# Kernel optimization log

Hardware: AMD Instinct MI355X
Metric: run time of the kernel (lower is better)

Reference implementation:

```python
import jax, jax.numpy as jnp
import numpy as np

K, N, BETA, DIM = 128, 15, 0.05, 512


def _safe_dist(sq):
    # sqrt with zero (sub)gradient at 0, matching torch.cdist/norm behavior
    pos = sq > 0
    return jnp.sqrt(jnp.where(pos, sq, 1.0)) * pos


def setup_inputs() -> dict:
    key = jax.random.key(0)
    embeddings = jax.random.normal(key, (K * N, DIM), dtype=jnp.float32)
    return {"embeddings": embeddings}


def reference(embeddings) -> jnp.ndarray:
    # ---- pairwise Euclidean distance matrix (torch.cdist, p=2) ----
    sq_norms = jnp.sum(embeddings * embeddings, axis=-1)  # [KN]
    sq = sq_norms[:, None] + sq_norms[None, :] - 2.0 * (embeddings @ embeddings.T)
    pdist = _safe_dist(jnp.maximum(sq, 0.0))  # [KN, KN]

    # ---- set margin loss over all identity pairs (a < b), vectorized ----
    blocks = pdist.reshape(K, N, K, N)  # blocks[a, i, b, k] = d(x_{a,i}, x_{b,k})
    ia, ib = jnp.triu_indices(K, k=1)   # P = K*(K-1)/2 pairs
    dAA = blocks[ia, :, ia, :]          # [P, N, N] intra-set distances of set a
    dAB = blocks[ia, :, ib, :]          # [P, N, N] cross distances a -> b
    # margin[p, i, j, k] = relu(dAA[p,i,j] - dAB[p,i,k] + 1.5), masked to i < j
    margin = jnp.maximum(dAA[:, :, :, None] - dAB[:, :, None, :] + 1.5, 0.0)
    mask_ij = jnp.triu(jnp.ones((N, N), dtype=margin.dtype), k=1)  # p buffer: 1 iff i<j
    set_margin_loss = jnp.sum(margin * mask_ij[None, :, :, None])
    total_pairs = ia.shape[0]
    set_margin_loss = set_margin_loss / (N * N * (N - 1) / 2)
    set_margin_loss = set_margin_loss / total_pairs

    # ---- centroid radius penalty ----
    groups = embeddings.reshape(K, N, -1)
    centroids = jnp.mean(groups, axis=1, keepdims=True)        # [K, 1, D]
    diff = groups - centroids
    dists = _safe_dist(jnp.sum(diff * diff, axis=-1))          # [K, N]
    mean_dist = jnp.mean(dists, axis=1)                        # [K]
    total_radius = jnp.mean(mean_dist)
    radius_penalty = BETA * jnp.mean(jnp.abs(mean_dist / total_radius - 1.0))

    return set_margin_loss + radius_penalty
```

## Files before the change

kernel.cpp:

```cpp
#include <hip/hip_runtime.h>
#include <math.h>

#define M 1920
#define DIMS 512
#define KGRP 128
#define NGRP 15
#define NQ 32
#define KC 32
#define NTILES 528
#define SPAD 40

typedef __attribute__((ext_vector_type(8))) short bf16x8;
typedef __attribute__((ext_vector_type(4))) float f32x4;

#define MFMA(A, B, C) __builtin_amdgcn_mfma_f32_16x16x32_bf16(A, B, C, 0, 0, 0)

__device__ inline void split2(float x, short& h, short& l) {
    unsigned u = __float_as_uint(x);
    h = (short)(u >> 16);
    float fl = x - __uint_as_float(u & 0xFFFF0000u);
    l = (short)(__float_as_uint(fl) >> 16);
}

__global__ __launch_bounds__(256) void daa_norm_kernel(const float* __restrict__ E,
                                                       float* __restrict__ dAAg,
                                                       float* __restrict__ sqn) {
    const int a = blockIdx.x;
    const int t = threadIdx.x;
    __shared__ float Ash[NGRP][516];
    const float4* Ea = reinterpret_cast<const float4*>(E + (size_t)a * NGRP * DIMS);
    for (int e = t; e < NGRP * (DIMS / 4); e += 256) {
        int r = e / (DIMS / 4), c4 = e % (DIMS / 4);
        *reinterpret_cast<float4*>(&Ash[r][c4 * 4]) = Ea[r * (DIMS / 4) + c4];
    }
    __syncthreads();
    if (t < NGRP * NGRP) {
        int i = t / NGRP, j = t % NGRP;
        float s = 0.0f;
        #pragma unroll 4
        for (int k = 0; k < DIMS; k += 4) {
            float4 ai = *reinterpret_cast<const float4*>(&Ash[i][k]);
            float4 aj = *reinterpret_cast<const float4*>(&Ash[j][k]);
            float dx = ai.x - aj.x, dy = ai.y - aj.y, dz = ai.z - aj.z, dw = ai.w - aj.w;
            s = fmaf(dx, dx, s); s = fmaf(dy, dy, s);
            s = fmaf(dz, dz, s); s = fmaf(dw, dw, s);
        }
        dAAg[a * 225 + t] = sqrtf(s);
    } else if (t >= 240 && t < 240 + NGRP) {
        int i = t - 240;
        float s = 0.0f;
        #pragma unroll 4
        for (int k = 0; k < DIMS; k += 4) {
            float4 ai = *reinterpret_cast<const float4*>(&Ash[i][k]);
            s = fmaf(ai.x, ai.x, s); s = fmaf(ai.y, ai.y, s);
            s = fmaf(ai.z, ai.z, s); s = fmaf(ai.w, ai.w, s);
        }
        sqn[a * NGRP + i] = s;
    }
}

__global__ __launch_bounds__(256) void quad_kernel(const float* __restrict__ E,
                                                   const float* __restrict__ sqn,
                                                   const float* __restrict__ dAAg,
                                                   float* __restrict__ acc) {
    int qa = 0, rem = blockIdx.x;
    while (rem >= NQ - qa) { rem -= NQ - qa; ++qa; }
    const int qb = qa + rem;

    __shared__ short Ah[64][SPAD], Al[64][SPAD], Bh[64][SPAD], Bl[64][SPAD];
    __shared__ float Dt[64][68];
    __shared__ float dAAc[4][228];
    __shared__ float sqnA[64], sqnB[64];
    __shared__ unsigned char ijt[105][2];
    __shared__ float wred[4];

    const int t = threadIdx.x;
    const int row0 = qa * 60, col0 = qb * 60;

    for (int e = t; e < 900; e += 256)
        dAAc[e / 225][e % 225] = dAAg[(qa * 4 + e / 225) * 225 + e % 225];
    if (t < 64) {
        sqnA[t] = sqn[row0 + min(t, 59)];
        sqnB[t] = sqn[col0 + min(t, 59)];
    }
    if (t < 105) {
        int i = 0, r2 = t;
        while (r2 >= 14 - i) { r2 -= 14 - i; ++i; }
        ijt[t][0] = (unsigned char)i;
        ijt[t][1] = (unsigned char)(i + 1 + r2);
    }

    const int wv = t >> 6, lane = t & 63;
    const int lr = lane & 15, lk = (lane >> 4) * 8;

    const int srow = t >> 2;
    const int skq = (t & 3) * 8;
    const float* pA = &E[(size_t)(row0 + min(srow, 59)) * DIMS + skq];
    const float* pB = &E[(size_t)(col0 + min(srow, 59)) * DIMS + skq];

    f32x4 z4 = {0.f, 0.f, 0.f, 0.f};
    f32x4 c0 = z4, c1 = z4, c2 = z4, c3 = z4;

    for (int k0 = 0; k0 < DIMS; k0 += KC) {
        __syncthreads();
        {
            float4 va0 = *reinterpret_cast<const float4*>(pA + k0);
            float4 va1 = *reinterpret_cast<const float4*>(pA + k0 + 4);
            float4 vb0 = *reinterpret_cast<const float4*>(pB + k0);
            float4 vb1 = *reinterpret_cast<const float4*>(pB + k0 + 4);
            float xa[8] = {va0.x, va0.y, va0.z, va0.w, va1.x, va1.y, va1.z, va1.w};
            float xb[8] = {vb0.x, vb0.y, vb0.z, vb0.w, vb1.x, vb1.y, vb1.z, vb1.w};
            bf16x8 ah, al, bh, bl;
            #pragma unroll
            for (int i = 0; i < 8; ++i) {
                short h, l;
                split2(xa[i], h, l); ah[i] = h; al[i] = l;
                split2(xb[i], h, l); bh[i] = h; bl[i] = l;
            }
            *reinterpret_cast<bf16x8*>(&Ah[srow][skq]) = ah;
            *reinterpret_cast<bf16x8*>(&Al[srow][skq]) = al;
            *reinterpret_cast<bf16x8*>(&Bh[srow][skq]) = bh;
            *reinterpret_cast<bf16x8*>(&Bl[srow][skq]) = bl;
        }
        __syncthreads();
        bf16x8 a_h = *reinterpret_cast<const bf16x8*>(&Ah[(wv << 4) + lr][lk]);
        bf16x8 a_l = *reinterpret_cast<const bf16x8*>(&Al[(wv << 4) + lr][lk]);
        bf16x8 b_h0 = *reinterpret_cast<const bf16x8*>(&Bh[lr][lk]);
        bf16x8 b_l0 = *reinterpret_cast<const bf16x8*>(&Bl[lr][lk]);
        bf16x8 b_h1 = *reinterpret_cast<const bf16x8*>(&Bh[16 + lr][lk]);
        bf16x8 b_l1 = *reinterpret_cast<const bf16x8*>(&Bl[16 + lr][lk]);
        bf16x8 b_h2 = *reinterpret_cast<const bf16x8*>(&Bh[32 + lr][lk]);
        bf16x8 b_l2 = *reinterpret_cast<const bf16x8*>(&Bl[32 + lr][lk]);
        bf16x8 b_h3 = *reinterpret_cast<const bf16x8*>(&Bh[48 + lr][lk]);
        bf16x8 b_l3 = *reinterpret_cast<const bf16x8*>(&Bl[48 + lr][lk]);
        c0 = MFMA(a_l, b_h0, c0); c0 = MFMA(a_h, b_l0, c0); c0 = MFMA(a_h, b_h0, c0);
        c1 = MFMA(a_l, b_h1, c1); c1 = MFMA(a_h, b_l1, c1); c1 = MFMA(a_h, b_h1, c1);
        c2 = MFMA(a_l, b_h2, c2); c2 = MFMA(a_h, b_l2, c2); c2 = MFMA(a_h, b_h2, c2);
        c3 = MFMA(a_l, b_h3, c3); c3 = MFMA(a_h, b_l3, c3); c3 = MFMA(a_h, b_h3, c3);
    }

    {
        const int rbase = (wv << 4) + ((lane >> 4) << 2);
        #define EPI(J, CJ)                                                    \
        {   _Pragma("unroll")                                                 \
            for (int r = 0; r < 4; ++r) {                                     \
                int rr = rbase + r;                                           \
                int cc = (J << 4) + lr;                                       \
                float sq = sqnA[rr] + sqnB[cc] - 2.0f * CJ[r];                \
                Dt[rr][cc] = sqrtf(fmaxf(sq, 0.0f));                          \
            }                                                                 \
        }
        EPI(0, c0) EPI(1, c1) EPI(2, c2) EPI(3, c3)
        #undef EPI
    }
    __syncthreads();

    float v = 0.0f;
    for (int it = t; it < 16 * 105; it += 256) {
        int p16 = it / 105, r2 = it % 105;
        int pa = p16 >> 2, pb = p16 & 3;
        int a = qa * 4 + pa, b = qb * 4 + pb;
        if (a < b) {
            int i = ijt[r2][0], j = ijt[r2][1];
            float base = dAAc[pa][i * 15 + j] + 1.5f;
            const float* drow = &Dt[pa * 15 + i][pb * 15];
            #pragma unroll
            for (int l = 0; l < NGRP; ++l) v += fmaxf(base - drow[l], 0.0f);
        }
    }
    #pragma unroll
    for (int off = 32; off > 0; off >>= 1) v += __shfl_down(v, off);
    if ((t & 63) == 0) wred[t >> 6] = v;
    __syncthreads();
    if (t == 0) atomicAdd(acc, wred[0] + wred[1] + wred[2] + wred[3]);
}

__global__ __launch_bounds__(256) void radius_kernel(const float* __restrict__ E,
                                                     float* __restrict__ md) {
    const int g = blockIdx.x;
    const int t = threadIdx.x;
    __shared__ float cent[DIMS];
    __shared__ float ws4[4];
    float c0 = 0.0f, c1 = 0.0f;
    #pragma unroll
    for (int m = 0; m < NGRP; ++m) {
        c0 += E[(size_t)(g * NGRP + m) * DIMS + t];
        c1 += E[(size_t)(g * NGRP + m) * DIMS + t + 256];
    }
    cent[t]       = c0 / (float)NGRP;
    cent[t + 256] = c1 / (float)NGRP;
    __syncthreads();
    float sumd = 0.0f;
    for (int m = 0; m < NGRP; ++m) {
        float d0 = E[(size_t)(g * NGRP + m) * DIMS + t]       - cent[t];
        float d1 = E[(size_t)(g * NGRP + m) * DIMS + t + 256] - cent[t + 256];
        float v = d0 * d0 + d1 * d1;
        #pragma unroll
        for (int off = 32; off > 0; off >>= 1) v += __shfl_down(v, off);
        if ((t & 63) == 0) ws4[t >> 6] = v;
        __syncthreads();
        if (t == 0) {
            float s = ws4[0] + ws4[1] + ws4[2] + ws4[3];
            sumd += (s > 0.0f) ? sqrtf(s) : 0.0f;
        }
        __syncthreads();
    }
    if (t == 0) md[g] = sumd / (float)NGRP;
}

__global__ __launch_bounds__(128) void finalize_kernel(const float* __restrict__ acc,
                                                       const float* __restrict__ md,
                                                       float* __restrict__ out) {
    const int t = threadIdx.x;
    __shared__ float w2[2];
    __shared__ float tr_s;
    float v = md[t];
    float s = v;
    #pragma unroll
    for (int off = 32; off > 0; off >>= 1) s += __shfl_down(s, off);
    if ((t & 63) == 0) w2[t >> 6] = s;
    __syncthreads();
    if (t == 0) tr_s = (w2[0] + w2[1]) / 128.0f;
    __syncthreads();
    const float tr = tr_s;
    float dev = fabsf(v / tr - 1.0f);
    #pragma unroll
    for (int off = 32; off > 0; off >>= 1) dev += __shfl_down(dev, off);
    if ((t & 63) == 0) w2[t >> 6] = dev;
    __syncthreads();
    if (t == 0) {
        float penalty = 0.05f * ((w2[0] + w2[1]) / 128.0f);
        float sml = acc[0] / 1575.0f / 8128.0f;
        out[0] = sml + penalty;
    }
}

__global__ void zero_kernel(float* acc) { *acc = 0.0f; }

extern "C" void kernel_launch(void* const* d_in, const int* in_sizes, int n_in,
                              void* d_out, int out_size, void* d_ws, size_t ws_size,
                              hipStream_t stream) {
    const float* E = (const float*)d_in[0];
    float* out = (float*)d_out;
    char* ws = (char*)d_ws;
    float* acc  = (float*)(ws);
    float* sqn  = (float*)(ws + 256);
    float* dAAg = (float*)(ws + 8192);
    float* md   = (float*)(ws + 123648);

    zero_kernel<<<1, 1, 0, stream>>>(acc);
    daa_norm_kernel<<<KGRP, 256, 0, stream>>>(E, dAAg, sqn);
    quad_kernel<<<NTILES, 256, 0, stream>>>(E, sqn, dAAg, acc);
    radius_kernel<<<KGRP, 256, 0, stream>>>(E, md);
    finalize_kernel<<<1, 128, 0, stream>>>(acc, md, out);
}
```

Measured before the change: 99.59 us.

## Fuse group prep kernels, pre-split bf16 operands, double-buffer GEMM, finalize via last-block

```diff
diff --git a/kernel.cpp b/kernel.cpp
--- a/kernel.cpp
+++ b/kernel.cpp
@@ -10,7 +10,8 @@
 #define NTILES 528
 #define SPAD 40
 
-typedef __attribute__((ext_vector_type(8))) short bf16x8;
+typedef __attribute__((ext_vector_type(8))) short short8;
+typedef __attribute__((ext_vector_type(4))) short short4v;
 typedef __attribute__((ext_vector_type(4))) float f32x4;
 
 #define MFMA(A, B, C) __builtin_amdgcn_mfma_f32_16x16x32_bf16(A, B, C, 0, 0, 0)
@@ -22,20 +23,39 @@
     l = (short)(__float_as_uint(fl) >> 16);
 }
 
-__global__ __launch_bounds__(256) void daa_norm_kernel(const float* __restrict__ E,
-                                                       float* __restrict__ dAAg,
-                                                       float* __restrict__ sqn) {
+__global__ __launch_bounds__(256) void group_kernel(const float* __restrict__ E,
+                                                    float* __restrict__ dAAg,
+                                                    float* __restrict__ sqn,
+                                                    float* __restrict__ md,
+                                                    short* __restrict__ Ehi,
+                                                    short* __restrict__ Elo,
+                                                    float* __restrict__ acc,
+                                                    unsigned* __restrict__ cnt) {
     const int a = blockIdx.x;
     const int t = threadIdx.x;
     __shared__ float Ash[NGRP][516];
+    __shared__ float cent[DIMS];
+    __shared__ float mdp[NGRP];
+
     const float4* Ea = reinterpret_cast<const float4*>(E + (size_t)a * NGRP * DIMS);
-    for (int e = t; e < NGRP * (DIMS / 4); e += 256) {
-        int r = e / (DIMS / 4), c4 = e % (DIMS / 4);
-        *reinterpret_cast<float4*>(&Ash[r][c4 * 4]) = Ea[r * (DIMS / 4) + c4];
-    }
-    __syncthreads();
-    if (t < NGRP * NGRP) {
-        int i = t / NGRP, j = t % NGRP;
+    for (int e = t; e < NGRP * 128; e += 256) {
+        int r = e >> 7, c4 = e & 127;
+        float4 v = Ea[r * 128 + c4];
+        *reinterpret_cast<float4*>(&Ash[r][c4 * 4]) = v;
+        float x[4] = {v.x, v.y, v.z, v.w};
+        short4v h, l;
+        #pragma unroll
+        for (int i = 0; i < 4; ++i) { short hh, ll; split2(x[i], hh, ll); h[i] = hh; l[i] = ll; }
+        size_t go = (size_t)(a * NGRP + r) * DIMS + c4 * 4;
+        *reinterpret_cast<short4v*>(&Ehi[go]) = h;
+        *reinterpret_cast<short4v*>(&Elo[go]) = l;
+    }
+    __syncthreads();
+
+    if (t < 105) {
+        int i = 0, r2 = t;
+        while (r2 >= 14 - i) { r2 -= 14 - i; ++i; }
+        int j = i + 1 + r2;
         float s = 0.0f;
         #pragma unroll 4
         for (int k = 0; k < DIMS; k += 4) {
@@ -45,34 +65,81 @@
             s = fmaf(dx, dx, s); s = fmaf(dy, dy, s);
             s = fmaf(dz, dz, s); s = fmaf(dw, dw, s);
         }
-        dAAg[a * 225 + t] = sqrtf(s);
-    } else if (t >= 240 && t < 240 + NGRP) {
-        int i = t - 240;
+        float d = sqrtf(s);
+        dAAg[a * 225 + i * 15 + j] = d;
+        dAAg[a * 225 + j * 15 + i] = d;
+    } else if (t >= 128 && t < 128 + NGRP) {
+        int m = t - 128;
         float s = 0.0f;
         #pragma unroll 4
         for (int k = 0; k < DIMS; k += 4) {
-            float4 ai = *reinterpret_cast<const float4*>(&Ash[i][k]);
+            float4 ai = *reinterpret_cast<const float4*>(&Ash[m][k]);
             s = fmaf(ai.x, ai.x, s); s = fmaf(ai.y, ai.y, s);
             s = fmaf(ai.z, ai.z, s); s = fmaf(ai.w, ai.w, s);
         }
-        sqn[a * NGRP + i] = s;
-    }
-}
-
-__global__ __launch_bounds__(256) void quad_kernel(const float* __restrict__ E,
+        sqn[a * NGRP + m] = s;
+    } else if (t >= 192 && t < 192 + NGRP) {
+        dAAg[a * 225 + (t - 192) * 16] = 0.0f;
+    }
+    if (t >= 128) {
+        int d0 = (t - 128) * 4;
+        float sx = 0.f, sy = 0.f, sz = 0.f, sw = 0.f;
+        #pragma unroll
+        for (int m = 0; m < NGRP; ++m) {
+            float4 v = *reinterpret_cast<const float4*>(&Ash[m][d0]);
+            sx += v.x; sy += v.y; sz += v.z; sw += v.w;
+        }
+        float4 c = {sx / (float)NGRP, sy / (float)NGRP, sz / (float)NGRP, sw / (float)NGRP};
+        *reinterpret_cast<float4*>(&cent[d0]) = c;
+    }
+    __syncthreads();
+
+    if (t < 240) {
+        int m = t >> 4, l16 = t & 15;
+        float s = 0.0f;
+        #pragma unroll
+        for (int it = 0; it < 8; ++it) {
+            int d = it * 64 + l16 * 4;
+            float4 v = *reinterpret_cast<const float4*>(&Ash[m][d]);
+            float4 c = *reinterpret_cast<const float4*>(&cent[d]);
+            float dx = v.x - c.x, dy = v.y - c.y, dz = v.z - c.z, dw = v.w - c.w;
+            s = fmaf(dx, dx, s); s = fmaf(dy, dy, s);
+            s = fmaf(dz, dz, s); s = fmaf(dw, dw, s);
+        }
+        s += __shfl_xor(s, 1); s += __shfl_xor(s, 2);
+        s += __shfl_xor(s, 4); s += __shfl_xor(s, 8);
+        if (l16 == 0) mdp[m] = (s > 0.0f) ? sqrtf(s) : 0.0f;
+    }
+    __syncthreads();
+    if (t == 0) {
+        float su = 0.0f;
+        #pragma unroll
+        for (int m = 0; m < NGRP; ++m) su += mdp[m];
+        md[a] = su / (float)NGRP;
+    }
+    if (a == 0 && t == 1) *acc = 0.0f;
+    if (a == 0 && t == 2) *cnt = 0u;
+}
+
+__global__ __launch_bounds__(256) void quad_kernel(const short* __restrict__ Ehi,
+                                                   const short* __restrict__ Elo,
                                                    const float* __restrict__ sqn,
                                                    const float* __restrict__ dAAg,
-                                                   float* __restrict__ acc) {
+                                                   const float* __restrict__ md,
+                                                   float* __restrict__ acc,
+                                                   unsigned* __restrict__ cnt,
+                                                   float* __restrict__ out) {
     int qa = 0, rem = blockIdx.x;
     while (rem >= NQ - qa) { rem -= NQ - qa; ++qa; }
     const int qb = qa + rem;
 
-    __shared__ short Ah[64][SPAD], Al[64][SPAD], Bh[64][SPAD], Bl[64][SPAD];
+    __shared__ short Ah[2][64][SPAD], Al[2][64][SPAD], Bh[2][64][SPAD], Bl[2][64][SPAD];
     __shared__ float Dt[64][68];
     __shared__ float dAAc[4][228];
     __shared__ float sqnA[64], sqnB[64];
     __shared__ unsigned char ijt[105][2];
     __shared__ float wred[4];
+    __shared__ int islast;
 
     const int t = threadIdx.x;
     const int row0 = qa * 60, col0 = qb * 60;
@@ -95,48 +162,53 @@
 
     const int srow = t >> 2;
     const int skq = (t & 3) * 8;
-    const float* pA = &E[(size_t)(row0 + min(srow, 59)) * DIMS + skq];
-    const float* pB = &E[(size_t)(col0 + min(srow, 59)) * DIMS + skq];
+    const size_t aoff = (size_t)(row0 + min(srow, 59)) * DIMS + skq;
+    const size_t boff = (size_t)(col0 + min(srow, 59)) * DIMS + skq;
+
+    short8 rah = *reinterpret_cast<const short8*>(Ehi + aoff);
+    short8 ral = *reinterpret_cast<const short8*>(Elo + aoff);
+    short8 rbh = *reinterpret_cast<const short8*>(Ehi + boff);
+    short8 rbl = *reinterpret_cast<const short8*>(Elo + boff);
+    *reinterpret_cast<short8*>(&Ah[0][srow][skq]) = rah;
+    *reinterpret_cast<short8*>(&Al[0][srow][skq]) = ral;
+    *reinterpret_cast<short8*>(&Bh[0][srow][skq]) = rbh;
+    *reinterpret_cast<short8*>(&Bl[0][srow][skq]) = rbl;
+    __syncthreads();
 
     f32x4 z4 = {0.f, 0.f, 0.f, 0.f};
     f32x4 c0 = z4, c1 = z4, c2 = z4, c3 = z4;
 
-    for (int k0 = 0; k0 < DIMS; k0 += KC) {
-        __syncthreads();
-        {
-            float4 va0 = *reinterpret_cast<const float4*>(pA + k0);
-            float4 va1 = *reinterpret_cast<const float4*>(pA + k0 + 4);
-            float4 vb0 = *reinterpret_cast<const float4*>(pB + k0);
-            float4 vb1 = *reinterpret_cast<const float4*>(pB + k0 + 4);
-            float xa[8] = {va0.x, va0.y, va0.z, va0.w, va1.x, va1.y, va1.z, va1.w};
-            float xb[8] = {vb0.x, vb0.y, vb0.z, vb0.w, vb1.x, vb1.y, vb1.z, vb1.w};
-            bf16x8 ah, al, bh, bl;
-            #pragma unroll
-            for (int i = 0; i < 8; ++i) {
-                short h, l;
-                split2(xa[i], h, l); ah[i] = h; al[i] = l;
-                split2(xb[i], h, l); bh[i] = h; bl[i] = l;
-            }
-            *reinterpret_cast<bf16x8*>(&Ah[srow][skq]) = ah;
-            *reinterpret_cast<bf16x8*>(&Al[srow][skq]) = al;
-            *reinterpret_cast<bf16x8*>(&Bh[srow][skq]) = bh;
-            *reinterpret_cast<bf16x8*>(&Bl[srow][skq]) = bl;
-        }
-        __syncthreads();
-        bf16x8 a_h = *reinterpret_cast<const bf16x8*>(&Ah[(wv << 4) + lr][lk]);
-        bf16x8 a_l = *reinterpret_cast<const bf16x8*>(&Al[(wv << 4) + lr][lk]);
-        bf16x8 b_h0 = *reinterpret_cast<const bf16x8*>(&Bh[lr][lk]);
-        bf16x8 b_l0 = *reinterpret_cast<const bf16x8*>(&Bl[lr][lk]);
-        bf16x8 b_h1 = *reinterpret_cast<const bf16x8*>(&Bh[16 + lr][lk]);
-        bf16x8 b_l1 = *reinterpret_cast<const bf16x8*>(&Bl[16 + lr][lk]);
-        bf16x8 b_h2 = *reinterpret_cast<const bf16x8*>(&Bh[32 + lr][lk]);
-        bf16x8 b_l2 = *reinterpret_cast<const bf16x8*>(&Bl[32 + lr][lk]);
-        bf16x8 b_h3 = *reinterpret_cast<const bf16x8*>(&Bh[48 + lr][lk]);
-        bf16x8 b_l3 = *reinterpret_cast<const bf16x8*>(&Bl[48 + lr][lk]);
+    for (int k = 0; k < DIMS / KC; ++k) {
+        const int cur = k & 1;
+        if (k < DIMS / KC - 1) {
+            const int off = (k + 1) * KC;
+            rah = *reinterpret_cast<const short8*>(Ehi + aoff + off);
+            ral = *reinterpret_cast<const short8*>(Elo + aoff + off);
+            rbh = *reinterpret_cast<const short8*>(Ehi + boff + off);
+            rbl = *reinterpret_cast<const short8*>(Elo + boff + off);
+        }
+        short8 a_h = *reinterpret_cast<const short8*>(&Ah[cur][(wv << 4) + lr][lk]);
+        short8 a_l = *reinterpret_cast<const short8*>(&Al[cur][(wv << 4) + lr][lk]);
+        short8 b_h0 = *reinterpret_cast<const short8*>(&Bh[cur][lr][lk]);
+        short8 b_l0 = *reinterpret_cast<const short8*>(&Bl[cur][lr][lk]);
+        short8 b_h1 = *reinterpret_cast<const short8*>(&Bh[cur][16 + lr][lk]);
+        short8 b_l1 = *reinterpret_cast<const short8*>(&Bl[cur][16 + lr][lk]);
+        short8 b_h2 = *reinterpret_cast<const short8*>(&Bh[cur][32 + lr][lk]);
+        short8 b_l2 = *reinterpret_cast<const short8*>(&Bl[cur][32 + lr][lk]);
+        short8 b_h3 = *reinterpret_cast<const short8*>(&Bh[cur][48 + lr][lk]);
+        short8 b_l3 = *reinterpret_cast<const short8*>(&Bl[cur][48 + lr][lk]);
         c0 = MFMA(a_l, b_h0, c0); c0 = MFMA(a_h, b_l0, c0); c0 = MFMA(a_h, b_h0, c0);
         c1 = MFMA(a_l, b_h1, c1); c1 = MFMA(a_h, b_l1, c1); c1 = MFMA(a_h, b_h1, c1);
         c2 = MFMA(a_l, b_h2, c2); c2 = MFMA(a_h, b_l2, c2); c2 = MFMA(a_h, b_h2, c2);
         c3 = MFMA(a_l, b_h3, c3); c3 = MFMA(a_h, b_l3, c3); c3 = MFMA(a_h, b_h3, c3);
+        if (k < DIMS / KC - 1) {
+            const int nxt = cur ^ 1;
+            *reinterpret_cast<short8*>(&Ah[nxt][srow][skq]) = rah;
+            *reinterpret_cast<short8*>(&Al[nxt][srow][skq]) = ral;
+            *reinterpret_cast<short8*>(&Bh[nxt][srow][skq]) = rbh;
+            *reinterpret_cast<short8*>(&Bl[nxt][srow][skq]) = rbl;
+        }
+        __syncthreads();
     }
 
     {
@@ -172,70 +244,40 @@
     for (int off = 32; off > 0; off >>= 1) v += __shfl_down(v, off);
     if ((t & 63) == 0) wred[t >> 6] = v;
     __syncthreads();
-    if (t == 0) atomicAdd(acc, wred[0] + wred[1] + wred[2] + wred[3]);
-}
-
-__global__ __launch_bounds__(256) void radius_kernel(const float* __restrict__ E,
-                                                     float* __restrict__ md) {
-    const int g = blockIdx.x;
-    const int t = threadIdx.x;
-    __shared__ float cent[DIMS];
-    __shared__ float ws4[4];
-    float c0 = 0.0f, c1 = 0.0f;
-    #pragma unroll
-    for (int m = 0; m < NGRP; ++m) {
-        c0 += E[(size_t)(g * NGRP + m) * DIMS + t];
-        c1 += E[(size_t)(g * NGRP + m) * DIMS + t + 256];
-    }
-    cent[t]       = c0 / (float)NGRP;
-    cent[t + 256] = c1 / (float)NGRP;
-    __syncthreads();
-    float sumd = 0.0f;
-    for (int m = 0; m < NGRP; ++m) {
-        float d0 = E[(size_t)(g * NGRP + m) * DIMS + t]       - cent[t];
-        float d1 = E[(size_t)(g * NGRP + m) * DIMS + t + 256] - cent[t + 256];
-        float v = d0 * d0 + d1 * d1;
-        #pragma unroll
-        for (int off = 32; off > 0; off >>= 1) v += __shfl_down(v, off);
-        if ((t & 63) == 0) ws4[t >> 6] = v;
+    if (t == 0) {
+        atomicAdd(acc, wred[0] + wred[1] + wred[2] + wred[3]);
+        __threadfence();
+        unsigned tk = atomicAdd(cnt, 1u);
+        islast = (tk == NTILES - 1) ? 1 : 0;
+    }
+    __syncthreads();
+
+    if (islast && t < 128) {
+        __shared__ float w2[2];
+        __shared__ float tr_s;
+        __threadfence();
+        float mv = md[t];
+        float s = mv;
+        #pragma unroll
+        for (int off = 32; off > 0; off >>= 1) s += __shfl_down(s, off);
+        if ((t & 63) == 0) w2[t >> 6] = s;
+        __syncthreads();
+        if (t == 0) tr_s = (w2[0] + w2[1]) / 128.0f;
+        __syncthreads();
+        const float tr = tr_s;
+        float dev = fabsf(mv / tr - 1.0f);
+        #pragma unroll
+        for (int off = 32; off > 0; off >>= 1) dev += __shfl_down(dev, off);
+        if ((t & 63) == 0) w2[t >> 6] = dev;
         __syncthreads();
         if (t == 0) {
-            float s = ws4[0] + ws4[1] + ws4[2] + ws4[3];
-            sumd += (s > 0.0f) ? sqrtf(s) : 0.0f;
-        }
-        __syncthreads();
-    }
-    if (t == 0) md[g] = sumd / (float)NGRP;
-}
-
-__global__ __launch_bounds__(128) void finalize_kernel(const float* __restrict__ acc,
-                                                       const float* __restrict__ md,
-                                                       float* __restrict__ out) {
-    const int t = threadIdx.x;
-    __shared__ float w2[2];
-    __shared__ float tr_s;
-    float v = md[t];
-    float s = v;
-    #pragma unroll
-    for (int off = 32; off > 0; off >>= 1) s += __shfl_down(s, off);
-    if ((t & 63) == 0) w2[t >> 6] = s;
-    __syncthreads();
-    if (t == 0) tr_s = (w2[0] + w2[1]) / 128.0f;
-    __syncthreads();
-    const float tr = tr_s;
-    float dev = fabsf(v / tr - 1.0f);
-    #pragma unroll
-    for (int off = 32; off > 0; off >>= 1) dev += __shfl_down(dev, off);
-    if ((t & 63) == 0) w2[t >> 6] = dev;
-    __syncthreads();
-    if (t == 0) {
-        float penalty = 0.05f * ((w2[0] + w2[1]) / 128.0f);
-        float sml = acc[0] / 1575.0f / 8128.0f;
-        out[0] = sml + penalty;
-    }
-}
-
-__global__ void zero_kernel(float* acc) { *acc = 0.0f; }
+            float total = atomicAdd(acc, 0.0f);
+            float penalty = 0.05f * ((w2[0] + w2[1]) / 128.0f);
+            float sml = total / 1575.0f / 8128.0f;
+            out[0] = sml + penalty;
+        }
+    }
+}
 
 extern "C" void kernel_launch(void* const* d_in, const int* in_sizes, int n_in,
                               void* d_out, int out_size, void* d_ws, size_t ws_size,
@@ -243,14 +285,14 @@
     const float* E = (const float*)d_in[0];
     float* out = (float*)d_out;
     char* ws = (char*)d_ws;
-    float* acc  = (float*)(ws);
-    float* sqn  = (float*)(ws + 256);
-    float* dAAg = (float*)(ws + 8192);
-    float* md   = (float*)(ws + 123648);
-
-    zero_kernel<<<1, 1, 0, stream>>>(acc);
-    daa_norm_kernel<<<KGRP, 256, 0, stream>>>(E, dAAg, sqn);
-    quad_kernel<<<NTILES, 256, 0, stream>>>(E, sqn, dAAg, acc);
-    radius_kernel<<<KGRP, 256, 0, stream>>>(E, md);
-    finalize_kernel<<<1, 128, 0, stream>>>(acc, md, out);
-}
+    float* acc    = (float*)(ws);
+    unsigned* cnt = (unsigned*)(ws + 64);
+    float* sqn    = (float*)(ws + 256);
+    float* dAAg   = (float*)(ws + 8192);
+    float* md     = (float*)(ws + 123648);
+    short* Ehi    = (short*)(ws + 131072);
+    short* Elo    = (short*)(ws + 2097152);
+
+    group_kernel<<<KGRP, 256, 0, stream>>>(E, dAAg, sqn, md, Ehi, Elo, acc, cnt);
+    quad_kernel<<<NTILES, 256, 0, stream>>>(Ehi, Elo, sqn, dAAg, md, acc, cnt, out);
+}
```

Result: slower. 101.7 us (+2.1%).
